# Optimization experiments

Measured on AMD Instinct MI355X. Metric: run time of the kernel, lower is better.

Reference implementation:

```python
import jax, jax.numpy as jnp
import numpy as np

N_ROWS = 100_000   # rows to encode
N_CLASSES = 1_000  # distinct classes C
N_WORDS = 8        # int32 words per string (32-char padded strings)
INT32_MIN = -(2**31)
INT32_MAX = 2**31 - 1


def setup_inputs() -> dict:
    key = jax.random.key(0)
    k_tab, k_idx = jax.random.split(key)
    # Class table: each row is a string packed into N_WORDS int32 words.
    # Random int32 rows are unique with overwhelming probability (256-bit keys).
    classes_table = jax.random.randint(
        k_tab, (N_CLASSES, N_WORDS), INT32_MIN, INT32_MAX, dtype=jnp.int32
    )
    # Every input row must be a previously-seen label: gather rows from the table.
    idx = jax.random.randint(k_idx, (N_ROWS,), 0, N_CLASSES)
    x = classes_table[idx]  # [N_ROWS, N_WORDS] int32
    return {"x": x, "classes_table": classes_table}


def reference(x, classes_table) -> jnp.ndarray:
    # torch: prod(condition_tensors == x.view(-1,1,L), dim=2).nonzero()[1]
    # Equality over all packed words == exact string match; exactly one class
    # matches each row, so argmax over the class dim recovers nonzero()[1].
    match = jnp.all(x[:, None, :] == classes_table[None, :, :], axis=2)  # [N, C] bool
    return jnp.argmax(match, axis=1).astype(jnp.int32)  # [N]
```

## Files before the change

### kernel.cpp

```cpp
#include <hip/hip_runtime.h>
#include <stdint.h>


#define N_ROWS    100000
#define N_CLASSES 1000
#define N_WORDS   8
#define TBL_SIZE  4096
#define TBL_MASK  (TBL_SIZE - 1)
#define BLOCK     256
#define ROWS_PER_THREAD 2
#define ROWS_PER_BLOCK  (BLOCK * ROWS_PER_THREAD)
#define NBLOCKS   ((N_ROWS + ROWS_PER_BLOCK - 1) / ROWS_PER_BLOCK)

__device__ __forceinline__ uint32_t hash8(int4 a, int4 b) {
    uint64_t h = 0x9E3779B97F4A7C15ull;
    uint32_t w[8] = {(uint32_t)a.x, (uint32_t)a.y, (uint32_t)a.z, (uint32_t)a.w,
                     (uint32_t)b.x, (uint32_t)b.y, (uint32_t)b.z, (uint32_t)b.w};
#pragma unroll
    for (int i = 0; i < 8; ++i) {
        h ^= w[i];
        h *= 0x100000001B3ull;
    }
    h ^= h >> 33;
    h *= 0xFF51AFD7ED558CCDull;
    h ^= h >> 33;
    return (uint32_t)h;
}

__global__ __launch_bounds__(BLOCK) void encode_fused(
        const int* __restrict__ x,
        const int* __restrict__ tab,
        int* __restrict__ out) {
    __shared__ int ht[TBL_SIZE];
    __shared__ int ctab[N_CLASSES * N_WORDS];

    const int t = threadIdx.x;

#pragma unroll
    for (int i = t; i < TBL_SIZE; i += BLOCK) ht[i] = -1;
    __syncthreads();

    for (int c = t; c < N_CLASSES; c += BLOCK) {
        const int4* t4 = (const int4*)(tab + (size_t)c * N_WORDS);
        int4 a = t4[0];
        int4 b = t4[1];
        ((int4*)ctab)[c * 2]     = a;
        ((int4*)ctab)[c * 2 + 1] = b;
        uint32_t h = hash8(a, b) & TBL_MASK;
        while (atomicCAS(&ht[h], -1, c) != -1) h = (h + 1) & TBL_MASK;
    }
    __syncthreads();

    const int base = blockIdx.x * ROWS_PER_BLOCK + t;
#pragma unroll
    for (int i = 0; i < ROWS_PER_THREAD; ++i) {
        int r = base + i * BLOCK;
        if (r >= N_ROWS) continue;
        const int4* x4 = (const int4*)(x + (size_t)r * N_WORDS);
        int4 a = x4[0];
        int4 b = x4[1];
        uint32_t h = hash8(a, b) & TBL_MASK;
        int res = 0;
        while (true) {
            int c = ht[h];
            if (c < 0) { res = 0; break; }
            int4 ta = ((const int4*)ctab)[c * 2];
            int4 tb = ((const int4*)ctab)[c * 2 + 1];
            if (ta.x == a.x && ta.y == a.y && ta.z == a.z && ta.w == a.w &&
                tb.x == b.x && tb.y == b.y && tb.z == b.z && tb.w == b.w) {
                res = c;
                break;
            }
            h = (h + 1) & TBL_MASK;
        }
        out[r] = res;
    }
}

extern "C" void kernel_launch(void* const* d_in, const int* in_sizes, int n_in,
                              void* d_out, int out_size, void* d_ws, size_t ws_size,
                              hipStream_t stream) {
    const int* x   = (const int*)d_in[0];
    const int* tab = (const int*)d_in[1];
    int* out = (int*)d_out;

    encode_fused<<<NBLOCKS, BLOCK, 0, stream>>>(x, tab, out);
}
```

Measured before the change: 61.17 us.

## Hash first word only, drop shared class copy, prefetch rows, one row per thread

Replaces the full 8-word FNV-style hash with a multiplicative hash of the first word, and stops copying the class table into shared memory; probes now verify matches by reading class rows from global memory through the cache. Each thread handles one row and issues its row load before the hash-table build so the load overlaps the setup. This shrinks shared memory per block, which can allow more resident blocks, and cuts hashing arithmetic. The cost is more blocks repeating the table build, global-memory reads on every probe, and more collisions if first words repeat.

```diff
diff --git a/kernel.cpp b/kernel.cpp
--- a/kernel.cpp
+++ b/kernel.cpp
@@ -8,23 +8,10 @@
 #define TBL_SIZE  4096
 #define TBL_MASK  (TBL_SIZE - 1)
 #define BLOCK     256
-#define ROWS_PER_THREAD 2
-#define ROWS_PER_BLOCK  (BLOCK * ROWS_PER_THREAD)
-#define NBLOCKS   ((N_ROWS + ROWS_PER_BLOCK - 1) / ROWS_PER_BLOCK)
+#define NBLOCKS   ((N_ROWS + BLOCK - 1) / BLOCK)
 
-__device__ __forceinline__ uint32_t hash8(int4 a, int4 b) {
-    uint64_t h = 0x9E3779B97F4A7C15ull;
-    uint32_t w[8] = {(uint32_t)a.x, (uint32_t)a.y, (uint32_t)a.z, (uint32_t)a.w,
-                     (uint32_t)b.x, (uint32_t)b.y, (uint32_t)b.z, (uint32_t)b.w};
-#pragma unroll
-    for (int i = 0; i < 8; ++i) {
-        h ^= w[i];
-        h *= 0x100000001B3ull;
-    }
-    h ^= h >> 33;
-    h *= 0xFF51AFD7ED558CCDull;
-    h ^= h >> 33;
-    return (uint32_t)h;
+__device__ __forceinline__ uint32_t hslot(uint32_t w0) {
+    return (w0 * 2654435761u) >> (32 - 12);
 }
 
 __global__ __launch_bounds__(BLOCK) void encode_fused(
@@ -32,49 +19,46 @@
         const int* __restrict__ tab,
         int* __restrict__ out) {
     __shared__ int ht[TBL_SIZE];
-    __shared__ int ctab[N_CLASSES * N_WORDS];
 
     const int t = threadIdx.x;
+    const int r = blockIdx.x * BLOCK + t;
+    const bool valid = (r < N_ROWS);
+
+    int4 a = {0, 0, 0, 0}, b = {0, 0, 0, 0};
+    if (valid) {
+        const int4* x4 = (const int4*)(x + (size_t)r * N_WORDS);
+        a = x4[0];
+        b = x4[1];
+    }
 
 #pragma unroll
     for (int i = t; i < TBL_SIZE; i += BLOCK) ht[i] = -1;
     __syncthreads();
 
     for (int c = t; c < N_CLASSES; c += BLOCK) {
-        const int4* t4 = (const int4*)(tab + (size_t)c * N_WORDS);
-        int4 a = t4[0];
-        int4 b = t4[1];
-        ((int4*)ctab)[c * 2]     = a;
-        ((int4*)ctab)[c * 2 + 1] = b;
-        uint32_t h = hash8(a, b) & TBL_MASK;
+        uint32_t h = hslot((uint32_t)tab[(size_t)c * N_WORDS]) & TBL_MASK;
         while (atomicCAS(&ht[h], -1, c) != -1) h = (h + 1) & TBL_MASK;
     }
     __syncthreads();
 
-    const int base = blockIdx.x * ROWS_PER_BLOCK + t;
-#pragma unroll
-    for (int i = 0; i < ROWS_PER_THREAD; ++i) {
-        int r = base + i * BLOCK;
-        if (r >= N_ROWS) continue;
-        const int4* x4 = (const int4*)(x + (size_t)r * N_WORDS);
-        int4 a = x4[0];
-        int4 b = x4[1];
-        uint32_t h = hash8(a, b) & TBL_MASK;
-        int res = 0;
-        while (true) {
-            int c = ht[h];
-            if (c < 0) { res = 0; break; }
-            int4 ta = ((const int4*)ctab)[c * 2];
-            int4 tb = ((const int4*)ctab)[c * 2 + 1];
-            if (ta.x == a.x && ta.y == a.y && ta.z == a.z && ta.w == a.w &&
-                tb.x == b.x && tb.y == b.y && tb.z == b.z && tb.w == b.w) {
-                res = c;
-                break;
-            }
-            h = (h + 1) & TBL_MASK;
+    if (!valid) return;
+
+    uint32_t h = hslot((uint32_t)a.x) & TBL_MASK;
+    int res = 0;
+    while (true) {
+        int c = ht[h];
+        if (c < 0) break;
+        const int4* t4 = (const int4*)(tab + (size_t)c * N_WORDS);
+        int4 ta = t4[0];
+        int4 tb = t4[1];
+        if (ta.x == a.x && ta.y == a.y && ta.z == a.z && ta.w == a.w &&
+            tb.x == b.x && tb.y == b.y && tb.z == b.z && tb.w == b.w) {
+            res = c;
+            break;
         }
-        out[r] = res;
+        h = (h + 1) & TBL_MASK;
     }
+    out[r] = res;
 }
 
 extern "C" void kernel_launch(void* const* d_in, const int* in_sizes, int n_in,
```

Result: no change. 60.17 us (-1.6%).
